# Kernel tuning notes

Measured on AMD Instinct MI355X. Metric: run time of the kernel, lower is better.

Reference implementation:

```python
import jax, jax.numpy as jnp
import numpy as np

B = 16384      # batch
IN = 512       # input width
G, F, O = 64, 24, 16      # hidden: groups, fan_in, group_out (width = G*O = 1024)
GO_G, GO_F, GO_O = 4, 48, 16  # output layer: 4 groups x 16 = 64 outputs


def setup_inputs() -> dict:
    key = jax.random.key(0)
    ks = jax.random.split(key, 13)
    # total columns available (concat of input + all prior hidden layers)
    tot = [IN, IN + G * O, IN + 2 * G * O, IN + 3 * G * O]  # 512,1536,2560,3584
    scale = 0.1
    return {
        "x": jax.random.normal(ks[0], (B, IN), jnp.float32),
        "W1": jax.random.normal(ks[1], (G, F, O), jnp.float32) * scale,
        "b1": jnp.zeros((G, O), jnp.float32),
        "W2": jax.random.normal(ks[2], (G, F, O), jnp.float32) * scale,
        "b2": jnp.zeros((G, O), jnp.float32),
        "W3": jax.random.normal(ks[3], (G, F, O), jnp.float32) * scale,
        "b3": jnp.zeros((G, O), jnp.float32),
        "Wo": jax.random.normal(ks[4], (GO_G, GO_F, GO_O), jnp.float32) * scale,
        "bo": jnp.zeros((GO_G, GO_O), jnp.float32),
        "idx1": jax.random.randint(ks[5], (G, F), 0, tot[0], jnp.int32),
        "idx2": jax.random.randint(ks[6], (G, F), 0, tot[1], jnp.int32),
        "idx3": jax.random.randint(ks[7], (G, F), 0, tot[2], jnp.int32),
        "idxo": jax.random.randint(ks[8], (GO_G, GO_F), 0, tot[3], jnp.int32),
    }


def _group_layer(acc, idx, W, b, act):
    # acc: [B, P] concat of all prior layer outputs; idx: [G, F] column coords
    g = acc[:, idx]                               # [B, G, F] irregular gather
    h = jnp.einsum('bgf,gfo->bgo', g, W) + b      # many tiny dense sublayers
    h = act(h)
    return h.reshape(h.shape[0], -1)              # concat groups -> [B, G*O]


def reference(x, W1, b1, W2, b2, W3, b3, Wo, bo, idx1, idx2, idx3, idxo):
    acc = x
    for idx, W, b in ((idx1, W1, b1), (idx2, W2, b2), (idx3, W3, b3)):
        out = _group_layer(acc, idx, W, b, jnp.tanh)
        acc = jnp.concatenate([acc, out], axis=1)  # inputs.append(layer_out)
    # output layer uses linear out_activation
    return _group_layer(acc, idxo, Wo, bo, lambda h: h)  # [B, 64]
```

## Files before the change

kernel.cpp:

```cpp
#include <hip/hip_runtime.h>
#include <hip/hip_bf16.h>


typedef unsigned short ushort_t;
typedef unsigned int uint_t;
typedef __attribute__((ext_vector_type(8))) short short8;
typedef __attribute__((ext_vector_type(4))) float f32x4;

#define ACC_STRIDE 3588
#define ROW_BYTES (ACC_STRIDE * 2)
#define PAD_ONE 3584
#define ONE_BYTE (PAD_ONE * 2)
#define ZERO_BYTE (3586 * 2)
#define ACC_U16 (16 * ACC_STRIDE)
#define OFFS_U16 6400
#define LDS_BYTES (ACC_U16 * 2 + OFFS_U16 * 2)

#define OFF_HIDO_B 204800
#define OFF_HEADO_B (204800 + 12288)

__device__ __forceinline__ ushort_t f2bf(float f) {
    __hip_bfloat16 h = __float2bfloat16(f);
    union { __hip_bfloat16 h; ushort_t u; } v;
    v.h = h;
    return v.u;
}

__device__ __forceinline__ uint_t pack2bf(float lo, float hi) {
    return (uint_t)f2bf(lo) | ((uint_t)f2bf(hi) << 16);
}

__device__ __forceinline__ float fast_tanh(float x) {
    float e = __expf(2.0f * x);
    return fmaf(-2.0f, __builtin_amdgcn_rcpf(e + 1.0f), 1.0f);
}

__device__ __forceinline__ void gather8(const char* accb, uint4 o, short8& af) {
    af[0] = *(const short*)(accb + (o.x & 0xffffu));
    af[1] = *(const short*)(accb + (o.x >> 16));
    af[2] = *(const short*)(accb + (o.y & 0xffffu));
    af[3] = *(const short*)(accb + (o.y >> 16));
    af[4] = *(const short*)(accb + (o.z & 0xffffu));
    af[5] = *(const short*)(accb + (o.z >> 16));
    af[6] = *(const short*)(accb + (o.w & 0xffffu));
    af[7] = *(const short*)(accb + (o.w >> 16));
}

__global__ __launch_bounds__(256)
void convert_weights(const float* __restrict__ W1, const float* __restrict__ b1,
                     const float* __restrict__ W2, const float* __restrict__ b2,
                     const float* __restrict__ W3, const float* __restrict__ b3,
                     const float* __restrict__ Wo, const float* __restrict__ bo,
                     const int* __restrict__ idx1, const int* __restrict__ idx2,
                     const int* __restrict__ idx3, const int* __restrict__ idxo,
                     ushort_t* __restrict__ ws)
{
    const int tid = blockIdx.x * 256 + threadIdx.x;
    const int lane = tid & 63;
    const int nn = lane & 15;
    const int quad = lane >> 4;
    if (tid < 12288) {
        const int g = (tid >> 6) & 63;
        const int l = tid >> 12;
        const float* W = (l == 0) ? W1 : (l == 1) ? W2 : W3;
        const float* bb = (l == 0) ? b1 : (l == 1) ? b2 : b3;
        const float* Wg = W + g * 384;
        ushort_t v[8];
        #pragma unroll
        for (int j = 0; j < 8; ++j) {
            const int k = quad * 8 + j;
            v[j] = (k < 24) ? f2bf(Wg[k * 16 + nn])
                 : (k == 24) ? f2bf(bb[g * 16 + nn]) : (ushort_t)0;
        }
        ushort4* dst = reinterpret_cast<ushort4*>(ws + (size_t)tid * 8);
        dst[0] = make_ushort4(v[0], v[1], v[2], v[3]);
        dst[1] = make_ushort4(v[4], v[5], v[6], v[7]);
    } else if (tid < 12800) {
        const int h = tid - 12288;
        const int gs = h >> 6;
        const int go = gs >> 1;
        const int step = gs & 1;
        const float* Wg = Wo + go * 768;
        ushort_t v[8];
        #pragma unroll
        for (int j = 0; j < 8; ++j) {
            const int k = step * 32 + quad * 8 + j;
            v[j] = (k < 48) ? f2bf(Wg[k * 16 + nn])
                 : (k == 48) ? f2bf(bo[go * 16 + nn]) : (ushort_t)0;
        }
        ushort4* dst = reinterpret_cast<ushort4*>(ws + (size_t)tid * 8);
        dst[0] = make_ushort4(v[0], v[1], v[2], v[3]);
        dst[1] = make_ushort4(v[4], v[5], v[6], v[7]);
    } else if (tid < 18944) {
        const int e = tid - 12800;
        const int l = e >> 11;
        const int rem = e & 2047;
        const int g = rem >> 5;
        const int k = rem & 31;
        const int* idx = (l == 0) ? idx1 : (l == 1) ? idx2 : idx3;
        const int v = (k < 24) ? idx[g * 24 + k] * 2
                    : (k == 24) ? ONE_BYTE : ZERO_BYTE;
        reinterpret_cast<ushort_t*>((char*)ws + OFF_HIDO_B)[e] = (ushort_t)v;
    } else if (tid < 19200) {
        const int e = tid - 18944;
        const int go = e >> 6;
        const int k = e & 63;
        const int v = (k < 48) ? idxo[go * 48 + k] * 2
                    : (k == 48) ? ONE_BYTE : ZERO_BYTE;
        reinterpret_cast<ushort_t*>((char*)ws + OFF_HEADO_B)[e] = (ushort_t)v;
    }
}

#define NTILES 4

__global__ __launch_bounds__(1024)
void demodel_mfma(const float* __restrict__ x,
                  const ushort_t* __restrict__ ws,
                  float* __restrict__ out)
{
    extern __shared__ __align__(16) ushort_t smem[];
    const int t = threadIdx.x;
    const int lane = t & 63;
    const int wv = t >> 6;
    const int nn = lane & 15;
    const int quad = lane >> 4;

    {
        const uint4* src = reinterpret_cast<const uint4*>((const char*)ws + OFF_HIDO_B);
        uint4* dst = reinterpret_cast<uint4*>(smem + ACC_U16);
        for (int i = t; i < (OFFS_U16 * 2) / 16; i += 1024)
            dst[i] = src[i];
    }
    if (t < 16) {
        uint2* p = reinterpret_cast<uint2*>((char*)smem + t * ROW_BYTES + ONE_BYTE);
        *p = make_uint2(0x00003f80u, 0u);
    }

    const ushort_t* offsu = smem + ACC_U16;
    const char* accb = (const char*)smem + nn * ROW_BYTES;
    char* accw = (char*)smem;

    const int pr = (t - 512) >> 5;
    const int pc = (t & 31) << 4;
    uint_t px[8];

    if (wv >= 8) {
        const float4* src = reinterpret_cast<const float4*>(
            x + ((size_t)blockIdx.x * 16 + pr) * 512 + pc);
        float4 a0 = src[0], a1 = src[1], a2 = src[2], a3 = src[3];
        px[0] = pack2bf(a0.x, a0.y); px[1] = pack2bf(a0.z, a0.w);
        px[2] = pack2bf(a1.x, a1.y); px[3] = pack2bf(a1.z, a1.w);
        px[4] = pack2bf(a2.x, a2.y); px[5] = pack2bf(a2.z, a2.w);
        px[6] = pack2bf(a3.x, a3.y); px[7] = pack2bf(a3.z, a3.w);
    }

    #pragma unroll 1
    for (int it = 0; it < NTILES; ++it) {
        const int row0 = (it * 256 + blockIdx.x) * 16;

        __syncthreads();
        if (wv >= 8) {
            uint2* d = reinterpret_cast<uint2*>(accw + pr * ROW_BYTES + pc * 2);
            d[0] = make_uint2(px[0], px[1]);
            d[1] = make_uint2(px[2], px[3]);
            d[2] = make_uint2(px[4], px[5]);
            d[3] = make_uint2(px[6], px[7]);
        }
        __syncthreads();

        #pragma unroll 1
        for (int l = 0; l < 3; ++l) {
            const int out_base = 512 + l * 1024;
            const int g0 = wv << 2;

            uint4 ofs[4];
            short8 bfr[4];
            #pragma unroll
            for (int gi = 0; gi < 4; ++gi) {
                ofs[gi] = *reinterpret_cast<const uint4*>(
                    offsu + l * 2048 + (g0 + gi) * 32 + quad * 8);
                bfr[gi] = *reinterpret_cast<const short8*>(
                    ws + (((size_t)l * 64 + g0 + gi) * 64 + lane) * 8);
            }

            short8 af[4];
            #pragma unroll
            for (int gi = 0; gi < 4; ++gi)
                gather8(accb, ofs[gi], af[gi]);

            f32x4 acc[4];
            #pragma unroll
            for (int gi = 0; gi < 4; ++gi) {
                f32x4 z = { 0.f, 0.f, 0.f, 0.f };
                acc[gi] = __builtin_amdgcn_mfma_f32_16x16x32_bf16(bfr[gi], af[gi], z, 0, 0, 0);
            }

            #pragma unroll
            for (int gi = 0; gi < 4; ++gi) {
                const int colo = out_base + (g0 + gi) * 16 + quad * 4;
                uint2 w = make_uint2(
                    pack2bf(fast_tanh(acc[gi][0]), fast_tanh(acc[gi][1])),
                    pack2bf(fast_tanh(acc[gi][2]), fast_tanh(acc[gi][3])));
                *reinterpret_cast<uint2*>(accw + nn * ROW_BYTES + colo * 2) = w;
            }
            __syncthreads();
        }

        if (wv < 4) {
            const int go = wv;
            uint4 ofs[2];
            short8 bfr[2];
            #pragma unroll
            for (int s = 0; s < 2; ++s) {
                ofs[s] = *reinterpret_cast<const uint4*>(
                    offsu + 6144 + go * 64 + s * 32 + quad * 8);
                bfr[s] = *reinterpret_cast<const short8*>(
                    ws + (12288 + ((size_t)go * 2 + s) * 64 + lane) * 8);
            }
            short8 af[2];
            #pragma unroll
            for (int s = 0; s < 2; ++s)
                gather8(accb, ofs[s], af[s]);
            f32x4 z = { 0.f, 0.f, 0.f, 0.f };
            f32x4 a0 = __builtin_amdgcn_mfma_f32_16x16x32_bf16(bfr[0], af[0], z, 0, 0, 0);
            f32x4 a1 = __builtin_amdgcn_mfma_f32_16x16x32_bf16(bfr[1], af[1], z, 0, 0, 0);
            float4 o;
            o.x = a0[0] + a1[0];
            o.y = a0[1] + a1[1];
            o.z = a0[2] + a1[2];
            o.w = a0[3] + a1[3];
            *reinterpret_cast<float4*>(
                out + (size_t)(row0 + nn) * 64 + go * 16 + quad * 4) = o;
        }
        if (wv >= 8 && it + 1 < NTILES) {
            const float4* src = reinterpret_cast<const float4*>(
                x + (((size_t)(it + 1) * 256 + blockIdx.x) * 16 + pr) * 512 + pc);
            float4 a0 = src[0], a1 = src[1], a2 = src[2], a3 = src[3];
            px[0] = pack2bf(a0.x, a0.y); px[1] = pack2bf(a0.z, a0.w);
            px[2] = pack2bf(a1.x, a1.y); px[3] = pack2bf(a1.z, a1.w);
            px[4] = pack2bf(a2.x, a2.y); px[5] = pack2bf(a2.z, a2.w);
            px[6] = pack2bf(a3.x, a3.y); px[7] = pack2bf(a3.z, a3.w);
        }
    }
}

extern "C" void kernel_launch(void* const* d_in, const int* in_sizes, int n_in,
                              void* d_out, int out_size, void* d_ws, size_t ws_size,
                              hipStream_t stream) {
    const float* x  = (const float*)d_in[0];
    const float* W1 = (const float*)d_in[1];
    const float* b1 = (const float*)d_in[2];
    const float* W2 = (const float*)d_in[3];
    const float* b2 = (const float*)d_in[4];
    const float* W3 = (const float*)d_in[5];
    const float* b3 = (const float*)d_in[6];
    const float* Wo = (const float*)d_in[7];
    const float* bo = (const float*)d_in[8];
    const int* idx1 = (const int*)d_in[9];
    const int* idx2 = (const int*)d_in[10];
    const int* idx3 = (const int*)d_in[11];
    const int* idxo = (const int*)d_in[12];
    float* out = (float*)d_out;

    (void)hipFuncSetAttribute((const void*)demodel_mfma,
                              hipFuncAttributeMaxDynamicSharedMemorySize,
                              LDS_BYTES);

    convert_weights<<<75, 256, 0, stream>>>(W1, b1, W2, b2, W3, b3, Wo, bo,
                                            idx1, idx2, idx3, idxo,
                                            (ushort_t*)d_ws);

    demodel_mfma<<<256, 1024, LDS_BYTES, stream>>>(
        x, (const ushort_t*)d_ws, out);
}
```

Measured before the change: 121.9 us.

## Unroll hidden layers, prefetch next-layer weights, and skip padded gather lanes

The three-layer loop is fully unrolled so the weights and offsets for the next layer are loaded before the current layer's tanh/write and barrier, hiding global and LDS latency. Lanes in quads that only cover padding (K beyond fan-in) skip the LDS gather and build a constant vector holding bf16 one for the bias slot instead of reading the stored one/zero columns. The output-layer loads are likewise hoisted ahead of the last barrier. This raises register pressure and depends on the padded offset layout matching the quad predicates.

```diff
diff --git a/kernel.cpp b/kernel.cpp
--- a/kernel.cpp
+++ b/kernel.cpp
@@ -18,6 +18,8 @@
 
 #define OFF_HIDO_B 204800
 #define OFF_HEADO_B (204800 + 12288)
+
+#define BF16_ONE ((short)0x3f80)
 
 __device__ __forceinline__ ushort_t f2bf(float f) {
     __hip_bfloat16 h = __float2bfloat16(f);
@@ -131,14 +133,11 @@
         for (int i = t; i < (OFFS_U16 * 2) / 16; i += 1024)
             dst[i] = src[i];
     }
-    if (t < 16) {
-        uint2* p = reinterpret_cast<uint2*>((char*)smem + t * ROW_BYTES + ONE_BYTE);
-        *p = make_uint2(0x00003f80u, 0u);
-    }
 
     const ushort_t* offsu = smem + ACC_U16;
     const char* accb = (const char*)smem + nn * ROW_BYTES;
     char* accw = (char*)smem;
+    const int g0 = wv << 2;
 
     const int pr = (t - 512) >> 5;
     const int pc = (t & 31) << 4;
@@ -154,6 +153,57 @@
         px[6] = pack2bf(a3.x, a3.y); px[7] = pack2bf(a3.z, a3.w);
     }
 
+#define LOAD_HIDDEN(L, OFS, BFR)                                            \
+    {                                                                       \
+        _Pragma("unroll")                                                   \
+        for (int gi = 0; gi < 4; ++gi)                                      \
+            BFR[gi] = *reinterpret_cast<const short8*>(                     \
+                ws + (((size_t)(L) * 64 + g0 + gi) * 64 + lane) * 8);       \
+        if (quad < 3) {                                                     \
+            _Pragma("unroll")                                               \
+            for (int gi = 0; gi < 4; ++gi)                                  \
+                OFS[gi] = *reinterpret_cast<const uint4*>(                  \
+                    offsu + (L) * 2048 + (g0 + gi) * 32 + quad * 8);        \
+        }                                                                   \
+    }
+
+#define GATHER_PRED(OFS, AF)                                                \
+    {                                                                       \
+        if (quad < 3) {                                                     \
+            _Pragma("unroll")                                               \
+            for (int gi = 0; gi < 4; ++gi) gather8(accb, OFS[gi], AF[gi]);  \
+        } else {                                                            \
+            _Pragma("unroll")                                               \
+            for (int gi = 0; gi < 4; ++gi) {                                \
+                short8 c = {};                                              \
+                c[0] = BF16_ONE;                                            \
+                AF[gi] = c;                                                 \
+            }                                                               \
+        }                                                                   \
+    }
+
+#define MFMA4(BFR, AF, ACC)                                                 \
+    {                                                                       \
+        _Pragma("unroll")                                                   \
+        for (int gi = 0; gi < 4; ++gi) {                                    \
+            f32x4 z = { 0.f, 0.f, 0.f, 0.f };                               \
+            ACC[gi] = __builtin_amdgcn_mfma_f32_16x16x32_bf16(              \
+                BFR[gi], AF[gi], z, 0, 0, 0);                               \
+        }                                                                   \
+    }
+
+#define WRITE_TANH(L, ACC)                                                  \
+    {                                                                       \
+        _Pragma("unroll")                                                   \
+        for (int gi = 0; gi < 4; ++gi) {                                    \
+            const int colo = 512 + (L) * 1024 + (g0 + gi) * 16 + quad * 4;  \
+            uint2 w = make_uint2(                                           \
+                pack2bf(fast_tanh(ACC[gi][0]), fast_tanh(ACC[gi][1])),      \
+                pack2bf(fast_tanh(ACC[gi][2]), fast_tanh(ACC[gi][3])));     \
+            *reinterpret_cast<uint2*>(accw + nn * ROW_BYTES + colo * 2) = w;\
+        }                                                                   \
+    }
+
     #pragma unroll 1
     for (int it = 0; it < NTILES; ++it) {
         const int row0 = (it * 256 + blockIdx.x) * 16;
@@ -166,71 +216,63 @@
             d[2] = make_uint2(px[4], px[5]);
             d[3] = make_uint2(px[6], px[7]);
         }
-        __syncthreads();
-
-        #pragma unroll 1
-        for (int l = 0; l < 3; ++l) {
-            const int out_base = 512 + l * 1024;
-            const int g0 = wv << 2;
-
-            uint4 ofs[4];
-            short8 bfr[4];
-            #pragma unroll
-            for (int gi = 0; gi < 4; ++gi) {
-                ofs[gi] = *reinterpret_cast<const uint4*>(
-                    offsu + l * 2048 + (g0 + gi) * 32 + quad * 8);
-                bfr[gi] = *reinterpret_cast<const short8*>(
-                    ws + (((size_t)l * 64 + g0 + gi) * 64 + lane) * 8);
+        uint4 ofsA[4]; short8 bfrA[4];
+        LOAD_HIDDEN(0, ofsA, bfrA)
+        __syncthreads();
+
+        short8 af[4];
+        f32x4 acc[4];
+        GATHER_PRED(ofsA, af)
+        MFMA4(bfrA, af, acc)
+        uint4 ofsB[4]; short8 bfrB[4];
+        LOAD_HIDDEN(1, ofsB, bfrB)
+        WRITE_TANH(0, acc)
+        __syncthreads();
+
+        GATHER_PRED(ofsB, af)
+        MFMA4(bfrB, af, acc)
+        LOAD_HIDDEN(2, ofsA, bfrA)
+        WRITE_TANH(1, acc)
+        __syncthreads();
+
+        GATHER_PRED(ofsA, af)
+        MFMA4(bfrA, af, acc)
+        uint4 hof0, hof1;
+        short8 hbf0, hbf1;
+        if (wv < 4) {
+            hof0 = *reinterpret_cast<const uint4*>(
+                offsu + 6144 + wv * 64 + quad * 8);
+            if (quad < 2)
+                hof1 = *reinterpret_cast<const uint4*>(
+                    offsu + 6144 + wv * 64 + 32 + quad * 8);
+            hbf0 = *reinterpret_cast<const short8*>(
+                ws + (12288 + ((size_t)wv * 2 + 0) * 64 + lane) * 8);
+            hbf1 = *reinterpret_cast<const short8*>(
+                ws + (12288 + ((size_t)wv * 2 + 1) * 64 + lane) * 8);
+        }
+        WRITE_TANH(2, acc)
+        __syncthreads();
+
+        if (wv < 4) {
+            short8 af0, af1;
+            gather8(accb, hof0, af0);
+            if (quad < 2) {
+                gather8(accb, hof1, af1);
+            } else {
+                short8 c = {};
+                if (quad == 2) c[0] = BF16_ONE;
+                af1 = c;
             }
-
-            short8 af[4];
-            #pragma unroll
-            for (int gi = 0; gi < 4; ++gi)
-                gather8(accb, ofs[gi], af[gi]);
-
-            f32x4 acc[4];
-            #pragma unroll
-            for (int gi = 0; gi < 4; ++gi) {
-                f32x4 z = { 0.f, 0.f, 0.f, 0.f };
-                acc[gi] = __builtin_amdgcn_mfma_f32_16x16x32_bf16(bfr[gi], af[gi], z, 0, 0, 0);
-            }
-
-            #pragma unroll
-            for (int gi = 0; gi < 4; ++gi) {
-                const int colo = out_base + (g0 + gi) * 16 + quad * 4;
-                uint2 w = make_uint2(
-                    pack2bf(fast_tanh(acc[gi][0]), fast_tanh(acc[gi][1])),
-                    pack2bf(fast_tanh(acc[gi][2]), fast_tanh(acc[gi][3])));
-                *reinterpret_cast<uint2*>(accw + nn * ROW_BYTES + colo * 2) = w;
-            }
-            __syncthreads();
-        }
-
-        if (wv < 4) {
-            const int go = wv;
-            uint4 ofs[2];
-            short8 bfr[2];
-            #pragma unroll
-            for (int s = 0; s < 2; ++s) {
-                ofs[s] = *reinterpret_cast<const uint4*>(
-                    offsu + 6144 + go * 64 + s * 32 + quad * 8);
-                bfr[s] = *reinterpret_cast<const short8*>(
-                    ws + (12288 + ((size_t)go * 2 + s) * 64 + lane) * 8);
-            }
-            short8 af[2];
-            #pragma unroll
-            for (int s = 0; s < 2; ++s)
-                gather8(accb, ofs[s], af[s]);
             f32x4 z = { 0.f, 0.f, 0.f, 0.f };
-            f32x4 a0 = __builtin_amdgcn_mfma_f32_16x16x32_bf16(bfr[0], af[0], z, 0, 0, 0);
-            f32x4 a1 = __builtin_amdgcn_mfma_f32_16x16x32_bf16(bfr[1], af[1], z, 0, 0, 0);
+            f32x4 a0 = __builtin_amdgcn_mfma_f32_16x16x32_bf16(hbf0, af0, z, 0, 0, 0);
+            f32x4 a1 = __builtin_amdgcn_mfma_f32_16x16x32_bf16(hbf1, af1, z, 0, 0, 0);
             float4 o;
             o.x = a0[0] + a1[0];
             o.y = a0[1] + a1[1];
             o.z = a0[2] + a1[2];
             o.w = a0[3] + a1[3];
             *reinterpret_cast<float4*>(
-                out + (size_t)(row0 + nn) * 64 + go * 16 + quad * 4) = o;
+                out + (size_t)(row0 + nn) * 64 + wv * 16 + quad * 4) = o;
         }
         if (wv >= 8 && it + 1 < NTILES) {
             const float4* src = reinterpret_cast<const float4*>(
@@ -242,6 +284,10 @@
             px[6] = pack2bf(a3.x, a3.y); px[7] = pack2bf(a3.z, a3.w);
         }
     }
+#undef LOAD_HIDDEN
+#undef GATHER_PRED
+#undef MFMA4
+#undef WRITE_TANH
 }
 
 extern "C" void kernel_launch(void* const* d_in, const int* in_sizes, int n_in,
```

New measurement: 144.6 us. +18.7%, slower.
